# Kernel optimization log

Hardware: AMD Instinct MI355X
Metric: run time of the kernel (lower is better)

## Reference

```python
import jax, jax.numpy as jnp
import numpy as np

B, T, C = 2, 2048, 1024
H = 16
D = C // H  # head_dim = 64
SCALE = D ** -0.5


def setup_inputs() -> dict:
    key = jax.random.key(0)
    ks = jax.random.split(key, 5)
    x = jax.random.normal(ks[0], (B, T, C), dtype=jnp.float32)
    # causal mask: -inf above diagonal, 0 elsewhere (module checks mask == -inf)
    neg_inf = jnp.float32(-jnp.inf)
    causal = jnp.where(jnp.tril(jnp.ones((T, T), dtype=bool)), 0.0, neg_inf)
    mask = causal[None, None, :, :].astype(jnp.float32)  # [1,1,T,T]
    # xavier_normal for [C, C] linear weights: std = sqrt(2/(C+C))
    std = float(np.sqrt(2.0 / (C + C)))
    wq = jax.random.normal(ks[1], (C, C), dtype=jnp.float32) * std
    wk = jax.random.normal(ks[2], (C, C), dtype=jnp.float32) * std
    wv = jax.random.normal(ks[3], (C, C), dtype=jnp.float32) * std
    wo = jax.random.normal(ks[4], (C, C), dtype=jnp.float32) * std
    return {"x": x, "mask": mask, "wq": wq, "wk": wk, "wv": wv, "wo": wo}


def reference(x, mask, wq, wk, wv, wo):
    # torch nn.Linear: y = x @ W.T
    q = jnp.einsum('btc,oc->bto', x, wq).reshape(B, T, H, D).transpose(0, 2, 1, 3)
    k = jnp.einsum('btc,oc->bto', x, wk).reshape(B, T, H, D).transpose(0, 2, 1, 3)
    v = jnp.einsum('btc,oc->bto', x, wv).reshape(B, T, H, D).transpose(0, 2, 1, 3)
    scores = jnp.einsum('bhqd,bhkd->bhqk', q, k) * SCALE  # [B,H,T,T]
    scores = jnp.where(mask == -jnp.inf, -jnp.inf, scores)
    attn = jax.nn.softmax(scores, axis=-1)
    out = jnp.einsum('bhqk,bhkd->bhqd', attn, v)  # [B,H,T,D]
    out = out.transpose(0, 2, 1, 3).reshape(B, T, C)
    return jnp.einsum('btc,oc->bto', out, wo)
```

## Files before the change

### kernel.cpp

```cpp
#include <hip/hip_runtime.h>
#include <hip/hip_bf16.h>


typedef __bf16 bf16_t;
typedef __bf16 bf16x8 __attribute__((ext_vector_type(8)));
typedef __bf16 bf16x4 __attribute__((ext_vector_type(4)));
typedef __bf16 bf16x2 __attribute__((ext_vector_type(2)));
typedef float  f32x4  __attribute__((ext_vector_type(4)));
typedef unsigned u32x4 __attribute__((ext_vector_type(4)));

__device__ __forceinline__ void gload_lds16(const bf16_t* g, bf16_t* l) {
  __builtin_amdgcn_global_load_lds((__attribute__((address_space(1))) void*)g,
                                   (__attribute__((address_space(3))) void*)l, 16, 0, 0);
}

__device__ __forceinline__ unsigned pack_bf16(float a, float b) {
  bf16x2 v; v[0] = (bf16_t)a; v[1] = (bf16_t)b;
  return __builtin_bit_cast(unsigned, v);
}

__global__ __launch_bounds__(256) void cvt_f32_bf16(const float* __restrict__ in,
                                                    bf16_t* __restrict__ out, int n4) {
  int i = blockIdx.x * 256 + threadIdx.x;
  if (i >= n4) return;
  float4 v = reinterpret_cast<const float4*>(in)[i];
  bf16x4 o;
  o[0] = (bf16_t)v.x; o[1] = (bf16_t)v.y; o[2] = (bf16_t)v.z; o[3] = (bf16_t)v.w;
  reinterpret_cast<bf16x4*>(out)[i] = o;
}

__global__ __launch_bounds__(256) void cvt_w4(const float* __restrict__ i0, const float* __restrict__ i1,
                                              const float* __restrict__ i2, const float* __restrict__ i3,
                                              bf16_t* __restrict__ o0, bf16_t* __restrict__ o1,
                                              bf16_t* __restrict__ o2, bf16_t* __restrict__ o3) {
  int which = blockIdx.y;
  const float* in = (which == 0) ? i0 : (which == 1) ? i1 : (which == 2) ? i2 : i3;
  bf16_t* out     = (which == 0) ? o0 : (which == 1) ? o1 : (which == 2) ? o2 : o3;
  int i = blockIdx.x * 256 + threadIdx.x;
  float4 v = reinterpret_cast<const float4*>(in)[i];
  bf16x4 o;
  o[0] = (bf16_t)v.x; o[1] = (bf16_t)v.y; o[2] = (bf16_t)v.z; o[3] = (bf16_t)v.w;
  reinterpret_cast<bf16x4*>(out)[i] = o;
}

#define TM 128
#define TN 128
#define TK 64

__global__ __launch_bounds__(256) void gemm_bt(
    const bf16_t* __restrict__ A,
    const bf16_t* __restrict__ W0, const bf16_t* __restrict__ W1, const bf16_t* __restrict__ W2,
    bf16_t* __restrict__ O0, bf16_t* __restrict__ O1, bf16_t* __restrict__ O2,
    float* __restrict__ OF, int kind)
{
  __shared__ alignas(16) bf16_t As[TM * TK];
  __shared__ alignas(16) bf16_t Bs[TN * TK];
  const int K = 1024;
  const int t = threadIdx.x;
  const int lane = t & 63;
  const int w = t >> 6;
  const int wr = w >> 1, wc = w & 1;
  const int lo = lane & 15, hi = lane >> 4;
  const int m0 = blockIdx.x * TM, n0 = blockIdx.y * TN;

  int mode;
  const bf16_t* Bw;
  bf16_t* outb = nullptr;
  if (kind == 1) { mode = 3; Bw = W0; }
  else {
    mode = blockIdx.z;
    Bw   = (mode == 0) ? W0 : (mode == 1) ? W1 : W2;
    outb = (mode == 0) ? O0 : (mode == 1) ? O1 : O2;
  }

  f32x4 acc[4][4] = {};
  const int srow = t >> 3;
  const int sch  = t & 7;

  for (int k0 = 0; k0 < K; k0 += TK) {
#pragma unroll
    for (int r = 0; r < 4; ++r) {
      int row = r * 32 + srow;
      gload_lds16(A  + (size_t)(m0 + row) * K + k0 + sch * 8, &As[row * TK + sch * 8]);
      gload_lds16(Bw + (size_t)(n0 + row) * K + k0 + sch * 8, &Bs[row * TK + sch * 8]);
    }
    __syncthreads();
#pragma unroll
    for (int ks = 0; ks < 2; ++ks) {
      bf16x8 af[4], bfr[4];
#pragma unroll
      for (int i = 0; i < 4; ++i) {
        af[i]  = *reinterpret_cast<const bf16x8*>(&As[(wr * 64 + i * 16 + lo) * TK + ks * 32 + hi * 8]);
        bfr[i] = *reinterpret_cast<const bf16x8*>(&Bs[(wc * 64 + i * 16 + lo) * TK + ks * 32 + hi * 8]);
      }
#pragma unroll
      for (int i = 0; i < 4; ++i)
#pragma unroll
        for (int j = 0; j < 4; ++j)
          acc[i][j] = __builtin_amdgcn_mfma_f32_16x16x32_bf16(af[i], bfr[j], acc[i][j], 0, 0, 0);
    }
    __syncthreads();
  }

#pragma unroll
  for (int i = 0; i < 4; ++i)
#pragma unroll
    for (int j = 0; j < 4; ++j)
#pragma unroll
      for (int r = 0; r < 4; ++r) {
        int m = m0 + wr * 64 + i * 16 + hi * 4 + r;
        int n = n0 + wc * 64 + j * 16 + lo;
        float v = acc[i][j][r];
        if (mode == 3) {
          OF[(size_t)m * 1024 + n] = v;
        } else {
          int b = m >> 11, tq = m & 2047;
          int h = n >> 6,  d  = n & 63;
          if (mode == 0) v *= 0.18033688011f;
          size_t addr = (mode == 2)
              ? ((size_t)(b * 16 + h) * 64 + d) * 2048 + tq
              : ((size_t)(b * 16 + h) * 2048 + tq) * 64 + d;
          outb[addr] = (bf16_t)v;
        }
      }
}

#define SLAB 8832

__global__ __launch_bounds__(256) void attn_fwd(
    const bf16_t* __restrict__ Q,
    const bf16_t* __restrict__ Km,
    const bf16_t* __restrict__ Vt,
    bf16_t* __restrict__ att)
{
  __shared__ alignas(16) char smem[4 * SLAB];
  const int t = threadIdx.x, lane = t & 63, w = t >> 6;
  const int lo = lane & 15, h = lane >> 4;
  const int item = blockIdx.x;
  const int bh = item >> 5;
  const int pr = item & 31;
  const bf16_t* Qb = Q  + (size_t)bh * 2048 * 64;
  const bf16_t* Kb = Km + (size_t)bh * 2048 * 64;
  const bf16_t* Vb = Vt + (size_t)bh * 64 * 2048;
  float* accW = (float*)(smem + w * SLAB);
  float* lW   = (float*)(smem + w * SLAB + 8704);
  const int b = bh >> 4, hd = bh & 15;
  const int src1 = lo + 32 * (h & 1);
  const int src2 = src1 + 16;
  const bool hsel = (h >> 1) != 0;

  auto run_tile = [&](int q0) {
    bf16x8 qf[2][2];
#pragma unroll
    for (int qt = 0; qt < 2; ++qt)
#pragma unroll
      for (int ks = 0; ks < 2; ++ks)
        qf[qt][ks] = *reinterpret_cast<const bf16x8*>(
            &Qb[(size_t)(q0 + qt * 16 + lo) * 64 + ks * 32 + h * 8]);

    f32x4 acc[2][4] = {};
    float lp[2] = {};
    const int kend = q0 + 32;
    for (int kb = w * 64; kb < kend; kb += 256) {
      f32x4 s_t[4][2] = {};
#pragma unroll
      for (int ks = 0; ks < 2; ++ks) {
        bf16x8 kf[4];
#pragma unroll
        for (int kt = 0; kt < 4; ++kt)
          kf[kt] = *reinterpret_cast<const bf16x8*>(
              &Kb[(size_t)(kb + kt * 16 + lo) * 64 + ks * 32 + h * 8]);
#pragma unroll
        for (int kt = 0; kt < 4; ++kt)
#pragma unroll
          for (int qt = 0; qt < 2; ++qt)
            s_t[kt][qt] = __builtin_amdgcn_mfma_f32_16x16x32_bf16(kf[kt], qf[qt][ks], s_t[kt][qt], 0, 0, 0);
      }
      bf16x8 vf[2][4];
#pragma unroll
      for (int kh = 0; kh < 2; ++kh)
#pragma unroll
        for (int dt = 0; dt < 4; ++dt)
          vf[kh][dt] = *reinterpret_cast<const bf16x8*>(
              &Vb[(size_t)(dt * 16 + lo) * 2048 + kb + kh * 32 + h * 8]);
      if (kb + 63 >= q0) {
#pragma unroll
        for (int kt = 0; kt < 4; ++kt)
#pragma unroll
          for (int qt = 0; qt < 2; ++qt)
#pragma unroll
            for (int r = 0; r < 4; ++r) {
              int kg = kb + kt * 16 + h * 4 + r;
              int qg = q0 + qt * 16 + lo;
              if (kg > qg) s_t[kt][qt][r] = -__builtin_inff();
            }
      }
      unsigned uP[2][4][2];
#pragma unroll
      for (int qt = 0; qt < 2; ++qt)
#pragma unroll
        for (int kt = 0; kt < 4; ++kt) {
          float p0 = exp2f(s_t[kt][qt][0]);
          float p1 = exp2f(s_t[kt][qt][1]);
          float p2 = exp2f(s_t[kt][qt][2]);
          float p3 = exp2f(s_t[kt][qt][3]);
          lp[qt] += (p0 + p1) + (p2 + p3);
          uP[qt][kt][0] = pack_bf16(p0, p1);
          uP[qt][kt][1] = pack_bf16(p2, p3);
        }
#pragma unroll
      for (int kh = 0; kh < 2; ++kh)
#pragma unroll
        for (int qt = 0; qt < 2; ++qt) {
          unsigned a0x = __shfl((int)uP[qt][2 * kh][0], src1);
          unsigned a0y = __shfl((int)uP[qt][2 * kh + 1][0], src1);
          unsigned a1x = __shfl((int)uP[qt][2 * kh][1], src1);
          unsigned a1y = __shfl((int)uP[qt][2 * kh + 1][1], src1);
          unsigned a2x = __shfl((int)uP[qt][2 * kh][0], src2);
          unsigned a2y = __shfl((int)uP[qt][2 * kh + 1][0], src2);
          unsigned a3x = __shfl((int)uP[qt][2 * kh][1], src2);
          unsigned a3y = __shfl((int)uP[qt][2 * kh + 1][1], src2);
          u32x4 au;
          au[0] = hsel ? a0y : a0x;
          au[1] = hsel ? a1y : a1x;
          au[2] = hsel ? a2y : a2x;
          au[3] = hsel ? a3y : a3x;
          bf16x8 pa = __builtin_bit_cast(bf16x8, au);
#pragma unroll
          for (int dt = 0; dt < 4; ++dt)
            acc[qt][dt] = __builtin_amdgcn_mfma_f32_16x16x32_bf16(pa, vf[kh][dt], acc[qt][dt], 0, 0, 0);
        }
    }

    float lrow[2];
#pragma unroll
    for (int qt = 0; qt < 2; ++qt) {
      float v = lp[qt];
      v += __shfl_xor(v, 16);
      v += __shfl_xor(v, 32);
      lrow[qt] = v;
    }

#pragma unroll
    for (int qt = 0; qt < 2; ++qt) {
#pragma unroll
      for (int r = 0; r < 4; ++r) {
        int row = qt * 16 + h * 4 + r;
#pragma unroll
        for (int dt = 0; dt < 4; ++dt)
          accW[row * 68 + dt * 16 + lo] = acc[qt][dt][r];
      }
      if (h == 0) lW[qt * 16 + lo] = lrow[qt];
    }
    __syncthreads();

    {
      const int row = t >> 3, c0 = (t & 7) * 8;
      float lsum = 0.f, o[8] = {};
#pragma unroll
      for (int w2 = 0; w2 < 4; ++w2) {
        lsum += ((const float*)(smem + w2 * SLAB + 8704))[row];
        const float* a2 = (const float*)(smem + w2 * SLAB) + row * 68 + c0;
#pragma unroll
        for (int j = 0; j < 8; ++j) o[j] += a2[j];
      }
      float inv = 1.f / lsum;
      bf16x8 ov;
#pragma unroll
      for (int j = 0; j < 8; ++j) ov[j] = (bf16_t)(o[j] * inv);
      *reinterpret_cast<bf16x8*>(&att[((size_t)(b * 2048 + q0 + row)) * 1024 + hd * 64 + c0]) = ov;
    }
    __syncthreads();
  };

  run_tile((63 - pr) * 32);
  run_tile(pr * 32);
}

extern "C" void kernel_launch(void* const* d_in, const int* in_sizes, int n_in,
                              void* d_out, int out_size, void* d_ws, size_t ws_size,
                              hipStream_t stream) {
  (void)in_sizes; (void)n_in; (void)out_size; (void)ws_size;
  const float* x  = (const float*)d_in[0];
  const float* wq = (const float*)d_in[2];
  const float* wk = (const float*)d_in[3];
  const float* wv = (const float*)d_in[4];
  const float* wo = (const float*)d_in[5];
  float* out = (float*)d_out;

  char* ws = (char*)d_ws;
  const size_t SZ_X = (size_t)4096 * 1024 * 2;
  const size_t SZ_W = (size_t)1024 * 1024 * 2;
  bf16_t* xb  = (bf16_t*)(ws);
  bf16_t* wqb = (bf16_t*)(ws + SZ_X);
  bf16_t* wkb = (bf16_t*)(ws + SZ_X + 1 * SZ_W);
  bf16_t* wvb = (bf16_t*)(ws + SZ_X + 2 * SZ_W);
  bf16_t* wob = (bf16_t*)(ws + SZ_X + 3 * SZ_W);
  bf16_t* qw  = (bf16_t*)(ws + 1 * SZ_X + 4 * SZ_W);
  bf16_t* kw  = (bf16_t*)(ws + 2 * SZ_X + 4 * SZ_W);
  bf16_t* vtw = (bf16_t*)(ws + 3 * SZ_X + 4 * SZ_W);
  bf16_t* att = xb;

  cvt_f32_bf16<<<4096, 256, 0, stream>>>(x, xb, 4096 * 1024 / 4);
  cvt_w4<<<dim3(1024, 4), 256, 0, stream>>>(wq, wk, wv, wo, wqb, wkb, wvb, wob);

  gemm_bt<<<dim3(32, 8, 3), 256, 0, stream>>>(xb, wqb, wkb, wvb, qw, kw, vtw, nullptr, 0);
  attn_fwd<<<1024, 256, 0, stream>>>(qw, kw, vtw, att);
  gemm_bt<<<dim3(32, 8, 1), 256, 0, stream>>>(att, wob, nullptr, nullptr,
                                              nullptr, nullptr, nullptr, out, 1);
}
```

Before: 169.2 us.

## Restructure attention to share K/V tiles in LDS across eight query waves

The attention kernel now runs 256 blocks of 512 threads. Each wave owns a 32-row query tile, and the block's eight waves share double-buffered K and V tiles staged through LDS with swizzled direct global-to-LDS loads. Before, each wave read K/V from global memory and split the key range across waves, which needed a cross-wave LDS reduction. Now each wave walks the full causal key range itself and writes its output directly. MFMA sections get raised priority. The risks are fewer blocks (256) for the GPU, causal load imbalance because blocks are ordered heaviest first by row group, and a barrier on every tile.

```diff
diff --git a/kernel.cpp b/kernel.cpp
--- a/kernel.cpp
+++ b/kernel.cpp
@@ -125,43 +125,64 @@
       }
 }
 
-#define SLAB 8832
-
-__global__ __launch_bounds__(256) void attn_fwd(
+__global__ __launch_bounds__(512) void attn_fwd(
     const bf16_t* __restrict__ Q,
     const bf16_t* __restrict__ Km,
     const bf16_t* __restrict__ Vt,
     bf16_t* __restrict__ att)
 {
-  __shared__ alignas(16) char smem[4 * SLAB];
+  __shared__ alignas(16) bf16_t Ks[2][64 * 64];
+  __shared__ alignas(16) bf16_t Vs[2][64 * 64];
   const int t = threadIdx.x, lane = t & 63, w = t >> 6;
   const int lo = lane & 15, h = lane >> 4;
-  const int item = blockIdx.x;
-  const int bh = item >> 5;
-  const int pr = item & 31;
+  const int blk = blockIdx.x;
+  const int a  = 7 - (blk >> 5);
+  const int bh = blk & 31;
+  const int q0 = 32 * (8 * a + w);
+  const int Rw = q0 + 32;
+  const int NT = 4 * (a + 1);
   const bf16_t* Qb = Q  + (size_t)bh * 2048 * 64;
   const bf16_t* Kb = Km + (size_t)bh * 2048 * 64;
   const bf16_t* Vb = Vt + (size_t)bh * 64 * 2048;
-  float* accW = (float*)(smem + w * SLAB);
-  float* lW   = (float*)(smem + w * SLAB + 8704);
   const int b = bh >> 4, hd = bh & 15;
   const int src1 = lo + 32 * (h & 1);
   const int src2 = src1 + 16;
   const bool hsel = (h >> 1) != 0;
 
-  auto run_tile = [&](int q0) {
-    bf16x8 qf[2][2];
-#pragma unroll
-    for (int qt = 0; qt < 2; ++qt)
-#pragma unroll
-      for (int ks = 0; ks < 2; ++ks)
-        qf[qt][ks] = *reinterpret_cast<const bf16x8*>(
-            &Qb[(size_t)(q0 + qt * 16 + lo) * 64 + ks * 32 + h * 8]);
-
-    f32x4 acc[2][4] = {};
-    float lp[2] = {};
-    const int kend = q0 + 32;
-    for (int kb = w * 64; kb < kend; kb += 256) {
+  const int sr = w * 8 + (lane >> 3);
+  const int sc = lane & 7;
+  const int scs = sc ^ (sr & 7);
+
+  auto stage = [&](int buf, int it) {
+    const int kb = it * 64;
+    gload_lds16(Kb + (size_t)(kb + sr) * 64 + scs * 8, &Ks[buf][sr * 64 + sc * 8]);
+    gload_lds16(Vb + (size_t)sr * 2048 + kb + scs * 8, &Vs[buf][sr * 64 + sc * 8]);
+  };
+
+  bf16x8 qf[2][2];
+#pragma unroll
+  for (int qt = 0; qt < 2; ++qt)
+#pragma unroll
+    for (int ks = 0; ks < 2; ++ks)
+      qf[qt][ks] = *reinterpret_cast<const bf16x8*>(
+          &Qb[(size_t)(q0 + qt * 16 + lo) * 64 + ks * 32 + h * 8]);
+
+  f32x4 acc[2][4] = {};
+  float lp[2] = {};
+
+  stage(0, 0);
+  for (int it = 0; it < NT; ++it) {
+    const int cur = it & 1;
+    if (it + 1 < NT) {
+      stage(cur ^ 1, it + 1);
+      asm volatile("s_waitcnt vmcnt(2)" ::: "memory");
+    } else {
+      asm volatile("s_waitcnt vmcnt(0)" ::: "memory");
+    }
+    __builtin_amdgcn_s_barrier();
+
+    const int kb = it * 64;
+    if (kb < Rw) {
       f32x4 s_t[4][2] = {};
 #pragma unroll
       for (int ks = 0; ks < 2; ++ks) {
@@ -169,20 +190,15 @@
 #pragma unroll
         for (int kt = 0; kt < 4; ++kt)
           kf[kt] = *reinterpret_cast<const bf16x8*>(
-              &Kb[(size_t)(kb + kt * 16 + lo) * 64 + ks * 32 + h * 8]);
+              &Ks[cur][(kt * 16 + lo) * 64 + ((ks * 4 + h) ^ (lo & 7)) * 8]);
+        __builtin_amdgcn_s_setprio(1);
 #pragma unroll
         for (int kt = 0; kt < 4; ++kt)
 #pragma unroll
           for (int qt = 0; qt < 2; ++qt)
             s_t[kt][qt] = __builtin_amdgcn_mfma_f32_16x16x32_bf16(kf[kt], qf[qt][ks], s_t[kt][qt], 0, 0, 0);
-      }
-      bf16x8 vf[2][4];
-#pragma unroll
-      for (int kh = 0; kh < 2; ++kh)
-#pragma unroll
-        for (int dt = 0; dt < 4; ++dt)
-          vf[kh][dt] = *reinterpret_cast<const bf16x8*>(
-              &Vb[(size_t)(dt * 16 + lo) * 2048 + kb + kh * 32 + h * 8]);
+        __builtin_amdgcn_s_setprio(0);
+      }
       if (kb + 63 >= q0) {
 #pragma unroll
         for (int kt = 0; kt < 4; ++kt)
@@ -209,7 +225,12 @@
           uP[qt][kt][1] = pack_bf16(p2, p3);
         }
 #pragma unroll
-      for (int kh = 0; kh < 2; ++kh)
+      for (int kh = 0; kh < 2; ++kh) {
+        bf16x8 vf[4];
+#pragma unroll
+        for (int dt = 0; dt < 4; ++dt)
+          vf[dt] = *reinterpret_cast<const bf16x8*>(
+              &Vs[cur][(dt * 16 + lo) * 64 + ((kh * 4 + h) ^ (lo & 7)) * 8]);
 #pragma unroll
         for (int qt = 0; qt < 2; ++qt) {
           unsigned a0x = __shfl((int)uP[qt][2 * kh][0], src1);
@@ -226,55 +247,36 @@
           au[2] = hsel ? a2y : a2x;
           au[3] = hsel ? a3y : a3x;
           bf16x8 pa = __builtin_bit_cast(bf16x8, au);
+          __builtin_amdgcn_s_setprio(1);
 #pragma unroll
           for (int dt = 0; dt < 4; ++dt)
-            acc[qt][dt] = __builtin_amdgcn_mfma_f32_16x16x32_bf16(pa, vf[kh][dt], acc[qt][dt], 0, 0, 0);
+            acc[qt][dt] = __builtin_amdgcn_mfma_f32_16x16x32_bf16(pa, vf[dt], acc[qt][dt], 0, 0, 0);
+          __builtin_amdgcn_s_setprio(0);
         }
-    }
-
-    float lrow[2];
-#pragma unroll
-    for (int qt = 0; qt < 2; ++qt) {
-      float v = lp[qt];
-      v += __shfl_xor(v, 16);
-      v += __shfl_xor(v, 32);
-      lrow[qt] = v;
-    }
-
-#pragma unroll
-    for (int qt = 0; qt < 2; ++qt) {
-#pragma unroll
-      for (int r = 0; r < 4; ++r) {
-        int row = qt * 16 + h * 4 + r;
-#pragma unroll
-        for (int dt = 0; dt < 4; ++dt)
-          accW[row * 68 + dt * 16 + lo] = acc[qt][dt][r];
-      }
-      if (h == 0) lW[qt * 16 + lo] = lrow[qt];
-    }
-    __syncthreads();
-
-    {
-      const int row = t >> 3, c0 = (t & 7) * 8;
-      float lsum = 0.f, o[8] = {};
-#pragma unroll
-      for (int w2 = 0; w2 < 4; ++w2) {
-        lsum += ((const float*)(smem + w2 * SLAB + 8704))[row];
-        const float* a2 = (const float*)(smem + w2 * SLAB) + row * 68 + c0;
-#pragma unroll
-        for (int j = 0; j < 8; ++j) o[j] += a2[j];
-      }
-      float inv = 1.f / lsum;
-      bf16x8 ov;
-#pragma unroll
-      for (int j = 0; j < 8; ++j) ov[j] = (bf16_t)(o[j] * inv);
-      *reinterpret_cast<bf16x8*>(&att[((size_t)(b * 2048 + q0 + row)) * 1024 + hd * 64 + c0]) = ov;
-    }
-    __syncthreads();
-  };
-
-  run_tile((63 - pr) * 32);
-  run_tile(pr * 32);
+      }
+    }
+    __builtin_amdgcn_s_barrier();
+  }
+
+  float lrow[2];
+#pragma unroll
+  for (int qt = 0; qt < 2; ++qt) {
+    float v = lp[qt];
+    v += __shfl_xor(v, 16);
+    v += __shfl_xor(v, 32);
+    lrow[qt] = v;
+  }
+#pragma unroll
+  for (int qt = 0; qt < 2; ++qt)
+#pragma unroll
+    for (int r = 0; r < 4; ++r) {
+      float inv = 1.f / __shfl(lrow[qt], h * 4 + r);
+      int tq = q0 + qt * 16 + h * 4 + r;
+#pragma unroll
+      for (int dt = 0; dt < 4; ++dt)
+        att[((size_t)(b * 2048 + tq)) * 1024 + hd * 64 + dt * 16 + lo] =
+            (bf16_t)(acc[qt][dt][r] * inv);
+    }
 }
 
 extern "C" void kernel_launch(void* const* d_in, const int* in_sizes, int n_in,
@@ -305,7 +307,7 @@
   cvt_w4<<<dim3(1024, 4), 256, 0, stream>>>(wq, wk, wv, wo, wqb, wkb, wvb, wob);
 
   gemm_bt<<<dim3(32, 8, 3), 256, 0, stream>>>(xb, wqb, wkb, wvb, qw, kw, vtw, nullptr, 0);
-  attn_fwd<<<1024, 256, 0, stream>>>(qw, kw, vtw, att);
+  attn_fwd<<<256, 512, 0, stream>>>(qw, kw, vtw, att);
   gemm_bt<<<dim3(32, 8, 1), 256, 0, stream>>>(att, wob, nullptr, nullptr,
                                               nullptr, nullptr, nullptr, out, 1);
 }
```

Measured after the change: 172.8 us. +2.2%, slower.
